# Optimization experiments

Hardware: AMD Instinct MI355X
Metric: run time of the kernel (lower is better)

The kernel has to match this reference:

```python
import jax, jax.numpy as jnp
import numpy as np

B, N, D, H = 32, 128, 64, 8
DH = D // H  # 8
LN_EPS = 1e-5


def _layer_norm(x, g, b):
    m = jnp.mean(x, axis=-1, keepdims=True)
    v = jnp.mean(jnp.square(x - m), axis=-1, keepdims=True)
    return (x - m) * jax.lax.rsqrt(v + LN_EPS) * g + b


def setup_inputs() -> dict:
    key = jax.random.key(0)
    ks = jax.random.split(key, 16)
    s = 0.05
    return {
        "h": jax.random.normal(ks[0], (B, N, D), jnp.float32),
        "p": jax.random.normal(ks[1], (B, N, D), jnp.float32),
        "e": jax.random.normal(ks[2], (B, N, N, D), jnp.float32),
        "k_RW": jax.random.uniform(ks[3], (B, N, N), jnp.float32),
        # projection weights stored as [in, out] (x @ W == torch Linear)
        "Wq": jax.random.normal(ks[4], (D, D), jnp.float32) * s,
        "Wk": jax.random.normal(ks[5], (D, D), jnp.float32) * s,
        "We": jax.random.normal(ks[6], (D, D), jnp.float32) * s,
        "Wv": jax.random.normal(ks[7], (D, D), jnp.float32) * s,
        "Wo": jax.random.normal(ks[8], (D, D), jnp.float32) * s,
        "bo": jnp.zeros((D,), jnp.float32),
        "ln1_g": jnp.ones((D,), jnp.float32),
        "ln1_b": jnp.zeros((D,), jnp.float32),
        "W1": jax.random.normal(ks[9], (D, 2 * D), jnp.float32) * s,
        "b1": jnp.zeros((2 * D,), jnp.float32),
        "W2": jax.random.normal(ks[10], (2 * D, D), jnp.float32) * s,
        "b2": jnp.zeros((D,), jnp.float32),
        "ln2_g": jnp.ones((D,), jnp.float32),
        "ln2_b": jnp.zeros((D,), jnp.float32),
    }


def reference(h, p, e, k_RW, Wq, Wk, We, Wv, Wo, bo, ln1_g, ln1_b, W1, b1, W2, b2, ln2_g, ln2_b):
    b, n, _ = h.shape
    Qh = (h @ Wq).reshape(b, n, H, DH)
    Kh = (h @ Wk).reshape(b, n, H, DH) * (DH ** -0.5)
    Vh = (h @ Wv).reshape(b, n, H, DH).transpose(0, 2, 1, 3)  # [b,h,n,d]
    E = (e @ We).reshape(b, n, n, H, DH)
    # edge-modulated scores: [b,h,i,j]
    scores = jnp.einsum('bihk,bjhk,bijhk->bhij', Qh, Kh, E)
    scores = jnp.exp(jnp.clip(scores, -5.0, 5.0))
    scores = scores * k_RW[:, None]  # adaptive edge PE scaling
    denom = jnp.maximum(scores.sum(-1, keepdims=True), 1e-6)
    attn = (scores @ Vh) / denom  # [b,h,n,d]
    attn = attn.transpose(0, 2, 1, 3).reshape(b, n, H * DH)
    h1 = h + (attn @ Wo + bo)  # residual + O projection
    h1 = _layer_norm(h1, ln1_g, ln1_b)
    ff = jax.nn.relu(h1 @ W1 + b1) @ W2 + b2
    h2 = _layer_norm(h1 + ff, ln2_g, ln2_b)
    return h2
```

## Files before the change

kernel.cpp:

```cpp
#include <hip/hip_runtime.h>


#define NB 32
#define NN 128
#define ND 64

typedef __attribute__((ext_vector_type(8))) __bf16 bf16x8;
typedef __attribute__((ext_vector_type(8))) unsigned short u16x8;
typedef __attribute__((ext_vector_type(4))) float f32x4;

static __device__ __forceinline__ unsigned short f2bf(float x) {
  unsigned u = __float_as_uint(x);
  u += 0x7fffu + ((u >> 16) & 1u);
  return (unsigned short)(u >> 16);
}

#define DPP_ADD(v, ctrl) \
  ((v) + __int_as_float(__builtin_amdgcn_update_dpp(0, __float_as_int(v), (ctrl), 0xf, 0xf, true)))

static __device__ __forceinline__ float wsum64(float v) {
  v += __shfl_xor(v, 1, 64);
  v += __shfl_xor(v, 2, 64);
  v += __shfl_xor(v, 4, 64);
  v += __shfl_xor(v, 8, 64);
  v += __shfl_xor(v, 16, 64);
  v += __shfl_xor(v, 32, 64);
  return v;
}

__global__ __launch_bounds__(64) void qkv_kernel(
    const float* __restrict__ h, const float* __restrict__ Wq,
    const float* __restrict__ Wk, const float* __restrict__ Wv,
    const float* __restrict__ We,
    float* __restrict__ Q, float* __restrict__ KT, float* __restrict__ V,
    unsigned short* __restrict__ WeT) {
  if (blockIdx.x == NB * NN) {
    const int t = threadIdx.x;
#pragma unroll
    for (int k0 = 0; k0 < ND; k0 += 8) {
      u16x8 u;
#pragma unroll
      for (int j = 0; j < 8; ++j) u[j] = f2bf(We[(k0 + j) * ND + t]);
      *(u16x8*)(&WeT[t * ND + k0]) = u;
    }
    return;
  }
  const int r = blockIdx.x;
  const int t = threadIdx.x;
  __shared__ float hrow[ND];
  hrow[t] = h[(size_t)r * ND + t];
  __syncthreads();
  float q = 0.f, k = 0.f, v = 0.f;
#pragma unroll 8
  for (int d = 0; d < ND; ++d) {
    const float hv = hrow[d];
    q = fmaf(hv, Wq[d * ND + t], q);
    k = fmaf(hv, Wk[d * ND + t], k);
    v = fmaf(hv, Wv[d * ND + t], v);
  }
  Q[(size_t)r * ND + t] = q;
  KT[((size_t)(r >> 7) * ND + t) * NN + (r & 127)] = k * 0.35355339059327373f;
  V[(size_t)r * ND + t] = v;
}

__global__ __launch_bounds__(64, 4) void fused_kernel(
    const float* __restrict__ h, const float* __restrict__ e,
    const float* __restrict__ kRW,
    const float* __restrict__ Wo, const float* __restrict__ bo,
    const float* __restrict__ g1, const float* __restrict__ be1,
    const float* __restrict__ W1, const float* __restrict__ b1,
    const float* __restrict__ W2, const float* __restrict__ b2,
    const float* __restrict__ g2, const float* __restrict__ be2,
    const float* __restrict__ Q, const float* __restrict__ KT,
    const float* __restrict__ V, const unsigned short* __restrict__ WeT,
    float* __restrict__ out) {
  const int blk = blockIdx.x;
  const int b = blk >> 7;
  const int i = blk & 127;
  const int L = threadIdx.x;
  const int quad = L >> 4;
  const int lrow = L & 15;
  const int h8 = L >> 3;

  __shared__ float S_lds[NN * 9];
  __shared__ float krw_lds[NN];
  __shared__ float q_lds[ND];
  __shared__ float attn_lds[ND];
  __shared__ float n1_lds[ND];
  __shared__ float ff_lds[2 * ND];

  const size_t row = (size_t)b * NN + i;
  const float* e_bi = e + row * (NN * ND);
  const size_t kvbase = (size_t)b * NN * ND;
  const size_t ktbase = (size_t)b * ND * NN;

  q_lds[L] = Q[row * ND + L];
  krw_lds[L] = kRW[row * NN + L];
  krw_lds[64 + L] = kRW[row * NN + 64 + L];

  bf16x8 bfr[2][4];
#pragma unroll
  for (int ks = 0; ks < 2; ++ks)
#pragma unroll
    for (int n0 = 0; n0 < 4; ++n0)
      bfr[ks][n0] = __builtin_bit_cast(
          bf16x8, *(const u16x8*)(&WeT[(n0 * 16 + lrow) * ND + ks * 32 + quad * 8]));

  __syncthreads();

#pragma unroll 2
  for (int mr = 0; mr < 8; ++mr) {
    const float* p = e_bi + (mr * 16 + lrow) * ND;
    bf16x8 afr[2];
#pragma unroll
    for (int ks = 0; ks < 2; ++ks) {
      const float4 v0 = *(const float4*)(p + ks * 32 + quad * 8);
      const float4 v1 = *(const float4*)(p + ks * 32 + quad * 8 + 4);
      u16x8 u;
      u[0] = f2bf(v0.x); u[1] = f2bf(v0.y); u[2] = f2bf(v0.z); u[3] = f2bf(v0.w);
      u[4] = f2bf(v1.x); u[5] = f2bf(v1.y); u[6] = f2bf(v1.z); u[7] = f2bf(v1.w);
      afr[ks] = __builtin_bit_cast(bf16x8, u);
    }
    f32x4 acc[4];
#pragma unroll
    for (int n0 = 0; n0 < 4; ++n0) acc[n0] = (f32x4){0.f, 0.f, 0.f, 0.f};
#pragma unroll
    for (int ks = 0; ks < 2; ++ks)
#pragma unroll
      for (int n0 = 0; n0 < 4; ++n0)
        acc[n0] = __builtin_amdgcn_mfma_f32_16x16x32_bf16(afr[ks], bfr[ks][n0], acc[n0], 0, 0, 0);

#pragma unroll
    for (int n0 = 0; n0 < 4; ++n0) {
      const int dout = n0 * 16 + lrow;
      const float qv = q_lds[dout];
      const float4 kv = *(const float4*)(&KT[ktbase + (size_t)dout * NN + mr * 16 + quad * 4]);
      const float* kvp = (const float*)&kv;
      float sv[4];
#pragma unroll
      for (int reg = 0; reg < 4; ++reg) {
        float tv = acc[n0][reg] * qv * kvp[reg];
        tv = DPP_ADD(tv, 0xB1);
        tv = DPP_ADD(tv, 0x4E);
        tv = DPP_ADD(tv, 0x141);
        sv[reg] = __expf(fminf(fmaxf(tv, -5.f), 5.f)) * krw_lds[mr * 16 + quad * 4 + reg];
      }
      if ((L & 7) == 0) {
#pragma unroll
        for (int reg = 0; reg < 4; ++reg)
          S_lds[(mr * 16 + quad * 4 + reg) * 9 + (dout >> 3)] = sv[reg];
      }
    }
  }
  __syncthreads();

  float nump = 0.f, denp = 0.f;
#pragma unroll 8
  for (int j = 0; j < NN; ++j) {
    const float s = S_lds[j * 9 + h8];
    const float v = V[kvbase + (size_t)j * ND + L];
    nump = fmaf(s, v, nump);
    denp += s;
  }
  attn_lds[L] = nump / fmaxf(denp, 1e-6f);
  __syncthreads();

  float o = bo[L];
#pragma unroll 8
  for (int d = 0; d < ND; ++d) o = fmaf(attn_lds[d], Wo[d * ND + L], o);
  const float h1v = h[row * ND + L] + o;
  const float m1 = wsum64(h1v) * (1.f / 64.f);
  const float df1 = h1v - m1;
  const float v1 = wsum64(df1 * df1) * (1.f / 64.f);
  const float n1 = df1 * rsqrtf(v1 + 1e-5f) * g1[L] + be1[L];
  n1_lds[L] = n1;
  __syncthreads();

  float a0 = b1[L], a1 = b1[64 + L];
#pragma unroll 8
  for (int d = 0; d < ND; ++d) {
    const float nv = n1_lds[d];
    a0 = fmaf(nv, W1[d * 128 + L], a0);
    a1 = fmaf(nv, W1[d * 128 + 64 + L], a1);
  }
  ff_lds[L] = fmaxf(a0, 0.f);
  ff_lds[64 + L] = fmaxf(a1, 0.f);
  __syncthreads();

  float o2 = b2[L];
#pragma unroll 8
  for (int u = 0; u < 128; ++u) o2 = fmaf(ff_lds[u], W2[u * ND + L], o2);
  const float x = n1 + o2;
  const float m2 = wsum64(x) * (1.f / 64.f);
  const float df2 = x - m2;
  const float v2 = wsum64(df2 * df2) * (1.f / 64.f);
  out[row * ND + L] = df2 * rsqrtf(v2 + 1e-5f) * g2[L] + be2[L];
}

extern "C" void kernel_launch(void* const* d_in, const int* in_sizes, int n_in,
                              void* d_out, int out_size, void* d_ws, size_t ws_size,
                              hipStream_t stream) {
  const float* h   = (const float*)d_in[0];
  const float* e   = (const float*)d_in[2];
  const float* kRW = (const float*)d_in[3];
  const float* Wq  = (const float*)d_in[4];
  const float* Wk  = (const float*)d_in[5];
  const float* We  = (const float*)d_in[6];
  const float* Wv  = (const float*)d_in[7];
  const float* Wo  = (const float*)d_in[8];
  const float* bo  = (const float*)d_in[9];
  const float* g1  = (const float*)d_in[10];
  const float* be1 = (const float*)d_in[11];
  const float* W1  = (const float*)d_in[12];
  const float* b1  = (const float*)d_in[13];
  const float* W2  = (const float*)d_in[14];
  const float* b2  = (const float*)d_in[15];
  const float* g2  = (const float*)d_in[16];
  const float* be2 = (const float*)d_in[17];
  float* out = (float*)d_out;

  float* Q  = (float*)d_ws;
  float* KT = Q + (size_t)NB * NN * ND;
  float* V  = KT + (size_t)NB * NN * ND;
  unsigned short* WeT = (unsigned short*)(V + (size_t)NB * NN * ND);

  qkv_kernel<<<NB * NN + 1, 64, 0, stream>>>(h, Wq, Wk, Wv, We, Q, KT, V, WeT);
  fused_kernel<<<NB * NN, 64, 0, stream>>>(h, e, kRW, Wo, bo, g1, be1,
                                           W1, b1, W2, b2, g2, be2, Q, KT, V, WeT, out);
}
```

Measured before the change: 258.0 us.

## Double-buffer edge and KT loads in registers and vectorize epilogue matvecs

The edge-tensor rows and KT tiles for the next two row blocks are prefetched into registers while the current block's MFMA and softmax work runs, so global load latency overlaps with compute. The score loop is fully unrolled and q/krw are hoisted out of it. The attention-V product and the Wo, W1 and W2 matvecs now use float4 loads, with each lane accumulating a partial sum over a subset of rows that is then combined with cross-lane shuffles. The occupancy hint in launch_bounds is dropped, which lets the compiler use more registers for the prefetch buffers at the possible cost of fewer resident waves.

```diff
diff --git a/kernel.cpp b/kernel.cpp
--- a/kernel.cpp
+++ b/kernel.cpp
@@ -28,6 +28,14 @@
   return v;
 }
 
+static __device__ __forceinline__ float4 xor_add4(float4 a, int m) {
+  a.x += __shfl_xor(a.x, m, 64);
+  a.y += __shfl_xor(a.y, m, 64);
+  a.z += __shfl_xor(a.z, m, 64);
+  a.w += __shfl_xor(a.w, m, 64);
+  return a;
+}
+
 __global__ __launch_bounds__(64) void qkv_kernel(
     const float* __restrict__ h, const float* __restrict__ Wq,
     const float* __restrict__ Wk, const float* __restrict__ Wv,
@@ -63,7 +71,7 @@
   V[(size_t)r * ND + t] = v;
 }
 
-__global__ __launch_bounds__(64, 4) void fused_kernel(
+__global__ __launch_bounds__(64) void fused_kernel(
     const float* __restrict__ h, const float* __restrict__ e,
     const float* __restrict__ kRW,
     const float* __restrict__ Wo, const float* __restrict__ bo,
@@ -79,8 +87,8 @@
   const int i = blk & 127;
   const int L = threadIdx.x;
   const int quad = L >> 4;
-  const int lrow = L & 15;
-  const int h8 = L >> 3;
+  const int c4 = L & 15;
+  const int lrow = c4;
 
   __shared__ float S_lds[NN * 9];
   __shared__ float krw_lds[NN];
@@ -106,21 +114,44 @@
       bfr[ks][n0] = __builtin_bit_cast(
           bf16x8, *(const u16x8*)(&WeT[(n0 * 16 + lrow) * ND + ks * 32 + quad * 8]));
 
-  __syncthreads();
-
-#pragma unroll 2
+  float4 eb[2][4], ktb[2][4];
+#define LD_E(mr, dst)                                              \
+  {                                                                \
+    const float* p_ = e_bi + ((mr) * 16 + lrow) * ND + quad * 8;   \
+    (dst)[0] = *(const float4*)(p_);                               \
+    (dst)[1] = *(const float4*)(p_ + 4);                           \
+    (dst)[2] = *(const float4*)(p_ + 32);                          \
+    (dst)[3] = *(const float4*)(p_ + 36);                          \
+  }
+#define LD_KT(mr, dst)                                                          \
+  {                                                                             \
+    _Pragma("unroll")                                                           \
+    for (int n0_ = 0; n0_ < 4; ++n0_)                                           \
+      (dst)[n0_] = *(const float4*)(&KT[ktbase + (size_t)(n0_ * 16 + lrow) * NN \
+                                        + (mr) * 16 + quad * 4]);               \
+  }
+  LD_E(0, eb[0]); LD_KT(0, ktb[0]);
+  LD_E(1, eb[1]); LD_KT(1, ktb[1]);
+  __syncthreads();
+
+  float qv[4];
+#pragma unroll
+  for (int n0 = 0; n0 < 4; ++n0) qv[n0] = q_lds[n0 * 16 + lrow];
+
+#pragma unroll
   for (int mr = 0; mr < 8; ++mr) {
-    const float* p = e_bi + (mr * 16 + lrow) * ND;
+    const int cur = mr & 1;
     bf16x8 afr[2];
 #pragma unroll
     for (int ks = 0; ks < 2; ++ks) {
-      const float4 v0 = *(const float4*)(p + ks * 32 + quad * 8);
-      const float4 v1 = *(const float4*)(p + ks * 32 + quad * 8 + 4);
+      const float4 v0 = eb[cur][ks * 2], v1 = eb[cur][ks * 2 + 1];
       u16x8 u;
       u[0] = f2bf(v0.x); u[1] = f2bf(v0.y); u[2] = f2bf(v0.z); u[3] = f2bf(v0.w);
       u[4] = f2bf(v1.x); u[5] = f2bf(v1.y); u[6] = f2bf(v1.z); u[7] = f2bf(v1.w);
       afr[ks] = __builtin_bit_cast(bf16x8, u);
     }
+    if (mr < 6) LD_E(mr + 2, eb[cur]);
+
     f32x4 acc[4];
 #pragma unroll
     for (int n0 = 0; n0 < 4; ++n0) acc[n0] = (f32x4){0.f, 0.f, 0.f, 0.f};
@@ -130,71 +161,141 @@
       for (int n0 = 0; n0 < 4; ++n0)
         acc[n0] = __builtin_amdgcn_mfma_f32_16x16x32_bf16(afr[ks], bfr[ks][n0], acc[n0], 0, 0, 0);
 
+    const float4 krw4 = *(const float4*)(&krw_lds[mr * 16 + quad * 4]);
+    const float* krwp = (const float*)&krw4;
 #pragma unroll
     for (int n0 = 0; n0 < 4; ++n0) {
-      const int dout = n0 * 16 + lrow;
-      const float qv = q_lds[dout];
-      const float4 kv = *(const float4*)(&KT[ktbase + (size_t)dout * NN + mr * 16 + quad * 4]);
-      const float* kvp = (const float*)&kv;
+      const float qn = qv[n0];
+      const float* kvp = (const float*)&ktb[cur][n0];
       float sv[4];
 #pragma unroll
       for (int reg = 0; reg < 4; ++reg) {
-        float tv = acc[n0][reg] * qv * kvp[reg];
+        float tv = acc[n0][reg] * qn * kvp[reg];
         tv = DPP_ADD(tv, 0xB1);
         tv = DPP_ADD(tv, 0x4E);
         tv = DPP_ADD(tv, 0x141);
-        sv[reg] = __expf(fminf(fmaxf(tv, -5.f), 5.f)) * krw_lds[mr * 16 + quad * 4 + reg];
+        sv[reg] = __expf(fminf(fmaxf(tv, -5.f), 5.f)) * krwp[reg];
       }
       if ((L & 7) == 0) {
+        const int hh = n0 * 2 + ((L >> 3) & 1);
 #pragma unroll
         for (int reg = 0; reg < 4; ++reg)
-          S_lds[(mr * 16 + quad * 4 + reg) * 9 + (dout >> 3)] = sv[reg];
+          S_lds[(mr * 16 + quad * 4 + reg) * 9 + hh] = sv[reg];
       }
     }
-  }
-  __syncthreads();
-
-  float nump = 0.f, denp = 0.f;
+    if (mr < 6) LD_KT(mr + 2, ktb[cur]);
+  }
+  __syncthreads();
+
+  const int jj = L >> 4;
+  const int hh2 = c4 >> 1;
+  float4 an = make_float4(0.f, 0.f, 0.f, 0.f);
+  float den = 0.f;
 #pragma unroll 8
-  for (int j = 0; j < NN; ++j) {
-    const float s = S_lds[j * 9 + h8];
-    const float v = V[kvbase + (size_t)j * ND + L];
-    nump = fmaf(s, v, nump);
-    denp += s;
-  }
-  attn_lds[L] = nump / fmaxf(denp, 1e-6f);
-  __syncthreads();
-
-  float o = bo[L];
+  for (int t = 0; t < 32; ++t) {
+    const int j = t * 4 + jj;
+    const float s = S_lds[j * 9 + hh2];
+    const float4 v = *(const float4*)(&V[kvbase + (size_t)j * ND + c4 * 4]);
+    an.x = fmaf(s, v.x, an.x);
+    an.y = fmaf(s, v.y, an.y);
+    an.z = fmaf(s, v.z, an.z);
+    an.w = fmaf(s, v.w, an.w);
+    den += s;
+  }
+  an = xor_add4(an, 16); an = xor_add4(an, 32);
+  den += __shfl_xor(den, 16, 64); den += __shfl_xor(den, 32, 64);
+  const float rden = 1.f / fmaxf(den, 1e-6f);
+  if (L < 16)
+    *(float4*)(&attn_lds[c4 * 4]) =
+        make_float4(an.x * rden, an.y * rden, an.z * rden, an.w * rden);
+  __syncthreads();
+
+  float4 o4 = make_float4(0.f, 0.f, 0.f, 0.f);
+#pragma unroll 4
+  for (int t = 0; t < 16; ++t) {
+    const int d = t * 4 + jj;
+    const float a = attn_lds[d];
+    const float4 wv = *(const float4*)(&Wo[d * ND + c4 * 4]);
+    o4.x = fmaf(a, wv.x, o4.x);
+    o4.y = fmaf(a, wv.y, o4.y);
+    o4.z = fmaf(a, wv.z, o4.z);
+    o4.w = fmaf(a, wv.w, o4.w);
+  }
+  o4 = xor_add4(o4, 16); o4 = xor_add4(o4, 32);
+  const float4 bo4 = *(const float4*)(&bo[c4 * 4]);
+  const float4 h4 = *(const float4*)(&h[row * ND + c4 * 4]);
+  float4 h1;
+  h1.x = h4.x + bo4.x + o4.x;
+  h1.y = h4.y + bo4.y + o4.y;
+  h1.z = h4.z + bo4.z + o4.z;
+  h1.w = h4.w + bo4.w + o4.w;
+  const float m1 = wsum64(h1.x + h1.y + h1.z + h1.w) * (1.f / 256.f);
+  float4 df;
+  df.x = h1.x - m1; df.y = h1.y - m1; df.z = h1.z - m1; df.w = h1.w - m1;
+  const float v1 =
+      wsum64(df.x * df.x + df.y * df.y + df.z * df.z + df.w * df.w) * (1.f / 256.f);
+  const float r1 = rsqrtf(v1 + 1e-5f);
+  const float4 g14 = *(const float4*)(&g1[c4 * 4]);
+  const float4 be14 = *(const float4*)(&be1[c4 * 4]);
+  float4 n14;
+  n14.x = df.x * r1 * g14.x + be14.x;
+  n14.y = df.y * r1 * g14.y + be14.y;
+  n14.z = df.z * r1 * g14.z + be14.z;
+  n14.w = df.w * r1 * g14.w + be14.w;
+  if (L < 16) *(float4*)(&n1_lds[c4 * 4]) = n14;
+  __syncthreads();
+
+  const int dd2 = L >> 5;
+  const int c5 = L & 31;
+  float4 f4 = make_float4(0.f, 0.f, 0.f, 0.f);
 #pragma unroll 8
-  for (int d = 0; d < ND; ++d) o = fmaf(attn_lds[d], Wo[d * ND + L], o);
-  const float h1v = h[row * ND + L] + o;
-  const float m1 = wsum64(h1v) * (1.f / 64.f);
-  const float df1 = h1v - m1;
-  const float v1 = wsum64(df1 * df1) * (1.f / 64.f);
-  const float n1 = df1 * rsqrtf(v1 + 1e-5f) * g1[L] + be1[L];
-  n1_lds[L] = n1;
-  __syncthreads();
-
-  float a0 = b1[L], a1 = b1[64 + L];
+  for (int t = 0; t < 32; ++t) {
+    const int d = t * 2 + dd2;
+    const float nv = n1_lds[d];
+    const float4 wv = *(const float4*)(&W1[d * 128 + c5 * 4]);
+    f4.x = fmaf(nv, wv.x, f4.x);
+    f4.y = fmaf(nv, wv.y, f4.y);
+    f4.z = fmaf(nv, wv.z, f4.z);
+    f4.w = fmaf(nv, wv.w, f4.w);
+  }
+  f4 = xor_add4(f4, 32);
+  const float4 b14 = *(const float4*)(&b1[c5 * 4]);
+  if (L < 32)
+    *(float4*)(&ff_lds[c5 * 4]) =
+        make_float4(fmaxf(f4.x + b14.x, 0.f), fmaxf(f4.y + b14.y, 0.f),
+                    fmaxf(f4.z + b14.z, 0.f), fmaxf(f4.w + b14.w, 0.f));
+  __syncthreads();
+
+  float4 q4 = make_float4(0.f, 0.f, 0.f, 0.f);
 #pragma unroll 8
-  for (int d = 0; d < ND; ++d) {
-    const float nv = n1_lds[d];
-    a0 = fmaf(nv, W1[d * 128 + L], a0);
-    a1 = fmaf(nv, W1[d * 128 + 64 + L], a1);
-  }
-  ff_lds[L] = fmaxf(a0, 0.f);
-  ff_lds[64 + L] = fmaxf(a1, 0.f);
-  __syncthreads();
-
-  float o2 = b2[L];
-#pragma unroll 8
-  for (int u = 0; u < 128; ++u) o2 = fmaf(ff_lds[u], W2[u * ND + L], o2);
-  const float x = n1 + o2;
-  const float m2 = wsum64(x) * (1.f / 64.f);
-  const float df2 = x - m2;
-  const float v2 = wsum64(df2 * df2) * (1.f / 64.f);
-  out[row * ND + L] = df2 * rsqrtf(v2 + 1e-5f) * g2[L] + be2[L];
+  for (int t = 0; t < 32; ++t) {
+    const int u = t * 4 + jj;
+    const float fv = ff_lds[u];
+    const float4 wv = *(const float4*)(&W2[u * ND + c4 * 4]);
+    q4.x = fmaf(fv, wv.x, q4.x);
+    q4.y = fmaf(fv, wv.y, q4.y);
+    q4.z = fmaf(fv, wv.z, q4.z);
+    q4.w = fmaf(fv, wv.w, q4.w);
+  }
+  q4 = xor_add4(q4, 16); q4 = xor_add4(q4, 32);
+  const float4 b24 = *(const float4*)(&b2[c4 * 4]);
+  float4 x4;
+  x4.x = n14.x + b24.x + q4.x;
+  x4.y = n14.y + b24.y + q4.y;
+  x4.z = n14.z + b24.z + q4.z;
+  x4.w = n14.w + b24.w + q4.w;
+  const float m2 = wsum64(x4.x + x4.y + x4.z + x4.w) * (1.f / 256.f);
+  float4 d2;
+  d2.x = x4.x - m2; d2.y = x4.y - m2; d2.z = x4.z - m2; d2.w = x4.w - m2;
+  const float v2 =
+      wsum64(d2.x * d2.x + d2.y * d2.y + d2.z * d2.z + d2.w * d2.w) * (1.f / 256.f);
+  const float r2 = rsqrtf(v2 + 1e-5f);
+  const float4 g24 = *(const float4*)(&g2[c4 * 4]);
+  const float4 be24 = *(const float4*)(&be2[c4 * 4]);
+  if (L < 16)
+    *(float4*)(&out[row * ND + c4 * 4]) =
+        make_float4(d2.x * r2 * g24.x + be24.x, d2.y * r2 * g24.y + be24.y,
+                    d2.z * r2 * g24.z + be24.z, d2.w * r2 * g24.w + be24.w);
 }
 
 extern "C" void kernel_launch(void* const* d_in, const int* in_sizes, int n_in,
```

Measured after the change: 256.5 us. Within noise of the previous version (-0.6%).
